# Kernel tuning notes

Measured on AMD Instinct MI355X. Metric: run time of the kernel, lower is better.

## Reference

```python
import math
import jax, jax.numpy as jnp
import numpy as np

WS = (2, 8, 8)   # (D, H, W) window
NUM_HEADS = 8


def get_position_index(ws):
    d, h, w = ws
    coords = jnp.stack(jnp.meshgrid(jnp.arange(d), jnp.arange(h), jnp.arange(w), indexing='ij'))
    cf = coords.reshape(3, -1)                      # [3, N]
    rel = cf[:, :, None] - cf[:, None, :]           # [3, N, N]
    rel = rel.transpose(1, 2, 0)                    # [N, N, 3]
    rel = rel + jnp.array([d - 1, h - 1, w - 1])
    rel = rel * jnp.array([(2 * h - 1) * (2 * w - 1), 2 * w - 1, 1])
    return rel.sum(-1)                              # [N, N] int32


def get_sine_position_encoding(HW, num_pos_feats, temperature=10000.0):
    # normalize=True path of the torch code
    scale = 2 * math.pi
    H, W = HW
    ones = jnp.ones((1, H, W), jnp.float32)
    y = jnp.cumsum(ones, 1)
    x = jnp.cumsum(ones, 2)
    eps = 1e-6
    y = y / (y[:, -1:, :] + eps) * scale
    x = x / (x[:, :, -1:] + eps) * scale
    dim_t = jnp.arange(num_pos_feats)
    dim_t = temperature ** (2.0 * (dim_t // 2).astype(jnp.float32) / num_pos_feats)
    px = x[..., None] / dim_t                       # [1,H,W,F]
    py = y[..., None] / dim_t
    px = jnp.stack((jnp.sin(px[..., 0::2]), jnp.cos(px[..., 1::2])), -1).reshape(1, H, W, num_pos_feats)
    py = jnp.stack((jnp.sin(py[..., 0::2]), jnp.cos(py[..., 1::2])), -1).reshape(1, H, W, num_pos_feats)
    pos = jnp.concatenate((py, px), 3)              # [1,H,W,2F]
    return pos.reshape(1, H * W, 2 * num_pos_feats)  # [1, H*W, C]


def setup_inputs() -> dict:
    key = jax.random.key(0)
    ks = jax.random.split(key, 6)
    B_, N, C = 2048, 128, 256
    return {
        'x': jax.random.normal(ks[0], (B_, N, C), jnp.float32),
        'rpb_table': jax.random.normal(ks[1], (675, NUM_HEADS), jnp.float32) * 0.02,
        'W_qkv_self': jax.random.normal(ks[2], (3 * C, C), jnp.float32) * 0.05,
        'W_qkv_mut': jax.random.normal(ks[3], (3 * C, C), jnp.float32) * 0.05,
        'W_proj': jax.random.normal(ks[4], (C, 2 * C), jnp.float32) * 0.05,
        'b_proj': jax.random.normal(ks[5], (C,), jnp.float32) * 0.05,
    }


def reference(x, rpb_table, W_qkv_self, W_qkv_mut, W_proj, b_proj):
    B, N, C = x.shape
    H = NUM_HEADS
    hd = C // H
    scale = hd ** -0.5

    def qkv_split(y, W):
        qkv = (y @ W.T).reshape(B, N, 3, H, hd).transpose(2, 0, 3, 1, 4)  # [3,B,H,N,hd]
        return qkv[0], qkv[1], qkv[2]

    def attn_fn(q, k, v, bias):
        a = jnp.einsum('bhnd,bhmd->bhnm', q * scale, k)
        if bias is not None:
            a = a + bias
        a = jax.nn.softmax(a, axis=-1)
        o = jnp.einsum('bhnm,bhmd->bhnd', a, v)
        return o.transpose(0, 2, 1, 3).reshape(B, -1, C)

    # self attention with relative position bias
    rpi = get_position_index(WS)                                   # [N,N]
    bias = rpb_table[rpi.reshape(-1)].reshape(N, N, H).transpose(2, 0, 1)[None]  # [1,H,N,N]
    q, k, v = qkv_split(x, W_qkv_self)
    x_out = attn_fn(q, k, v, bias)                                 # [B,N,C]

    # mutual cross-attention between the two frames
    pos = jnp.tile(get_sine_position_encoding(WS[1:], C // 2), (1, 2, 1)).astype(x.dtype)
    q, k, v = qkv_split(x + pos, W_qkv_mut)
    Nh = N // 2
    q1, q2 = q[:, :, :Nh], q[:, :, Nh:]
    k1, k2 = k[:, :, :Nh], k[:, :, Nh:]
    v1, v2 = v[:, :, :Nh], v[:, :, Nh:]
    x1_aligned = attn_fn(q2, k1, v1, None)                         # [B,N/2,C]
    x2_aligned = attn_fn(q1, k2, v2, None)
    x_out = jnp.concatenate([jnp.concatenate([x1_aligned, x2_aligned], 1), x_out], 2)  # [B,N,2C]

    return x_out @ W_proj.T + b_proj                               # [B,N,C]
```

## Files before the change

kernel.cpp:

```cpp
#include <hip/hip_runtime.h>


typedef __attribute__((ext_vector_type(8))) short     short8;
typedef __attribute__((ext_vector_type(8))) __bf16    bf16x8;
typedef __attribute__((ext_vector_type(4))) float     f32x4;

#define LOG2E 1.4426950408889634f

__device__ __forceinline__ unsigned short f2bf(float f) {
  return __builtin_bit_cast(unsigned short, (__bf16)f);
}

__device__ __forceinline__ void gload_lds16(const void* g, void* l) {
  __builtin_amdgcn_global_load_lds((const __attribute__((address_space(1))) void*)g,
                                   (__attribute__((address_space(3))) void*)l, 16, 0, 0);
}


__global__ void pos_kernel(float* __restrict__ pos_t) {
  int e = blockIdx.x * 256 + threadIdx.x;
  int t = e >> 8, c = e & 255;
  int p = t & 63;
  const float norm = 6.28318530717958647692f / 8.000001f;
  float yn = (float)((p >> 3) + 1) * norm;
  float xn = (float)((p & 7) + 1) * norm;
  int cc = c & 127;
  int m  = cc >> 1;
  float v = ((c < 128) ? yn : xn) * __expf(-(float)m * 0.14391156831f);
  pos_t[e] = (cc & 1) ? cosf(v) : sinf(v);
}

__global__ void posw_kernel(const float* __restrict__ pos_t,
                            const float* __restrict__ Wm,
                            float* __restrict__ posW) {
  int e = blockIdx.x * 256 + threadIdx.x;
  int t = e / 768, c = e - t * 768;
  const float4* pr = (const float4*)(pos_t + t * 256);
  const float4* wr = (const float4*)(Wm + (size_t)c * 256);
  float acc = 0.f;
  #pragma unroll 8
  for (int k = 0; k < 64; ++k) {
    float4 p = pr[k], w = wr[k];
    acc += p.x * w.x + p.y * w.y + p.z * w.z + p.w * w.w;
  }
  if (c < 256) acc *= 0.17677669529663688f * LOG2E;
  posW[e] = acc;
}

__global__ void bias_kernel(const float* __restrict__ rpb, float* __restrict__ bias_t) {
  int e = blockIdx.x * 256 + threadIdx.x;
  int h = e >> 14, i = (e >> 7) & 127, j = e & 127;
  int di = i >> 6, hi = (i >> 3) & 7, wi = i & 7;
  int dj = j >> 6, hj = (j >> 3) & 7, wj = j & 7;
  int idx = (di - dj + 1) * 225 + (hi - hj + 7) * 15 + (wi - wj + 7);
  bias_t[e] = rpb[idx * 8 + h] * LOG2E;
}

__global__ void wconv_kernel(const float* __restrict__ Ws, const float* __restrict__ Wm,
                             const float* __restrict__ Wp,
                             unsigned short* __restrict__ Wsb,
                             unsigned short* __restrict__ Wmb,
                             unsigned short* __restrict__ Wpb) {
  int e = blockIdx.x * 256 + threadIdx.x;
  const float qs = 0.17677669529663688f * LOG2E;
  if (e < 196608) {
    float v = Ws[e]; if (e < 65536) v *= qs;
    Wsb[e] = f2bf(v);
  } else if (e < 393216) {
    int i = e - 196608;
    float v = Wm[i]; if (i < 65536) v *= qs;
    Wmb[i] = f2bf(v);
  } else {
    Wpb[e - 393216] = f2bf(Wp[e - 393216]);
  }
}

__global__ void xconv_kernel(const float* __restrict__ x, unsigned short* __restrict__ xb16) {
  for (size_t i8 = ((size_t)blockIdx.x * 256 + threadIdx.x) * 8; i8 < 67108864ull;
       i8 += (size_t)gridDim.x * 256 * 8) {
    float4 a = *(const float4*)(x + i8);
    float4 d = *(const float4*)(x + i8 + 4);
    short8 o;
    o[0] = (short)f2bf(a.x); o[1] = (short)f2bf(a.y);
    o[2] = (short)f2bf(a.z); o[3] = (short)f2bf(a.w);
    o[4] = (short)f2bf(d.x); o[5] = (short)f2bf(d.y);
    o[6] = (short)f2bf(d.z); o[7] = (short)f2bf(d.w);
    *(short8*)(xb16 + i8) = o;
  }
}


template<bool XB>
__global__ __launch_bounds__(512, 4) void qkv_attn(
    const float* __restrict__ xf,
    const unsigned short* __restrict__ xb16,
    const unsigned short* __restrict__ Wsb,
    const unsigned short* __restrict__ Wmb,
    const float* __restrict__ posW,
    const float* __restrict__ bias_t,
    unsigned short* __restrict__ xcat)
{
  __shared__ unsigned short Wl[24576];
  __shared__ unsigned short Qsh[128 * 40];
  __shared__ unsigned short Ksh[128 * 40];
  __shared__ unsigned short VT[32 * 136];
  unsigned short* Psh = Wl;

  const int kblk = blockIdx.x;
  const int b    = (kblk & 7) | ((kblk >> 7) << 3);
  const int g    = (kblk >> 3) & 15;
  const int h    = g >> 1;
  const bool self = (g & 1) == 0;

  const int tid = threadIdx.x, w = tid >> 6, lane = tid & 63;
  const int lr = lane & 15, lk = lane >> 4;
  const unsigned short* Wb = self ? Wsb : Wmb;
  const int m0 = w * 16;

  #pragma unroll
  for (int i = 0; i < 6; ++i) {
    int s  = w * 6 + i;
    int u  = s >> 3, kc = s & 7;
    int o  = u >> 1, nt = u & 1;
    gload_lds16((const char*)Wb + (size_t)(o * 256 + h * 32 + nt * 16 + lr) * 512
                                + kc * 64 + lk * 16,
                (char*)Wl + s * 1024 + lane * 16);
  }

  float pre_r[32];
  if (self) {
    const float* bt = bias_t + (size_t)h * 16384 + (m0 + lk * 4) * 128;
    #pragma unroll
    for (int nf = 0; nf < 8; ++nf)
      #pragma unroll
      for (int r = 0; r < 4; ++r)
        pre_r[nf * 4 + r] = bt[r * 128 + nf * 16 + lr];
  } else {
    #pragma unroll
    for (int u = 0; u < 6; ++u) {
      const int o = u >> 1, nt = u & 1;
      #pragma unroll
      for (int r = 0; r < 4; ++r)
        pre_r[u * 4 + r] = posW[(m0 + lk * 4 + r) * 768 + o * 256 + h * 32 + nt * 16 + lr];
    }
  }

  const float*          xrowf = xf   + (size_t)((b * 128 + m0 + lr) * 256 + lk * 8);
  const unsigned short* xrowb = xb16 + (size_t)((b * 128 + m0 + lr) * 256 + lk * 8);

  float4 xrf[2][2];
  short8 xrb[2];
  if (XB) {
    xrb[0] = *(const short8*)(xrowb);
    xrb[1] = *(const short8*)(xrowb + 32);
  } else {
    xrf[0][0] = *(const float4*)(xrowf);
    xrf[0][1] = *(const float4*)(xrowf + 4);
    xrf[1][0] = *(const float4*)(xrowf + 32);
    xrf[1][1] = *(const float4*)(xrowf + 36);
  }

  __syncthreads();

  f32x4 acc[6];
  #pragma unroll
  for (int u = 0; u < 6; ++u) acc[u] = f32x4{0.f, 0.f, 0.f, 0.f};

  const char* wfrag = (const char*)Wl + lane * 16;

  #pragma unroll
  for (int kc = 0; kc < 8; ++kc) {
    bf16x8 af;
    if (XB) {
      af = __builtin_bit_cast(bf16x8, xrb[kc & 1]);
      if (kc + 2 < 8) xrb[kc & 1] = *(const short8*)(xrowb + (kc + 2) * 32);
    } else {
      float4 a = xrf[kc & 1][0], d = xrf[kc & 1][1];
      if (kc + 2 < 8) {
        xrf[kc & 1][0] = *(const float4*)(xrowf + (kc + 2) * 32);
        xrf[kc & 1][1] = *(const float4*)(xrowf + (kc + 2) * 32 + 4);
      }
      af[0] = (__bf16)a.x; af[1] = (__bf16)a.y; af[2] = (__bf16)a.z; af[3] = (__bf16)a.w;
      af[4] = (__bf16)d.x; af[5] = (__bf16)d.y; af[6] = (__bf16)d.z; af[7] = (__bf16)d.w;
    }
    __builtin_amdgcn_s_setprio(1);
    #pragma unroll
    for (int u = 0; u < 6; ++u) {
      bf16x8 wf = *(const bf16x8*)(wfrag + ((u * 8 + kc) << 10));
      acc[u] = __builtin_amdgcn_mfma_f32_16x16x32_bf16(af, wf, acc[u], 0, 0, 0);
    }
    __builtin_amdgcn_s_setprio(0);
  }

  #pragma unroll
  for (int u = 0; u < 6; ++u) {
    const int o = u >> 1, nt = u & 1;
    #pragma unroll
    for (int r = 0; r < 4; ++r) {
      int row  = m0 + lk * 4 + r;
      int dcol = nt * 16 + lr;
      float v = acc[u][r];
      if (!self) v += pre_r[u * 4 + r];
      if (o == 2)      VT[dcol * 136 + row] = f2bf(v);
      else if (o == 0) Qsh[row * 40 + dcol] = f2bf(v);
      else             Ksh[row * 40 + dcol] = f2bf(v);
    }
  }
  __syncthreads();

  if (self) {
    f32x4 sc[8];
    bf16x8 qa = *(const bf16x8*)&Qsh[(m0 + lr) * 40 + lk * 8];
    __builtin_amdgcn_s_setprio(1);
    #pragma unroll
    for (int nf = 0; nf < 8; ++nf) {
      bf16x8 kb = *(const bf16x8*)&Ksh[(nf * 16 + lr) * 40 + lk * 8];
      sc[nf] = __builtin_amdgcn_mfma_f32_16x16x32_bf16(qa, kb,
                                                       f32x4{0.f,0.f,0.f,0.f}, 0, 0, 0);
    }
    __builtin_amdgcn_s_setprio(0);
    float rsum[4] = {0.f, 0.f, 0.f, 0.f};
    #pragma unroll
    for (int nf = 0; nf < 8; ++nf)
      #pragma unroll
      for (int r = 0; r < 4; ++r) {
        float p = exp2f(sc[nf][r] + pre_r[nf * 4 + r]);
        rsum[r] += p;
        sc[nf][r] = p;
      }
    float rs[4];
    #pragma unroll
    for (int r = 0; r < 4; ++r) {
      float t = rsum[r];
      #pragma unroll
      for (int dd = 1; dd < 16; dd <<= 1) t += __shfl_xor(t, dd, 64);
      rs[r] = 1.f / t;
    }
    f32x4 oc[2];
    oc[0] = f32x4{0.f,0.f,0.f,0.f}; oc[1] = f32x4{0.f,0.f,0.f,0.f};
    #pragma unroll
    for (int c = 0; c < 4; ++c) {
      #pragma unroll
      for (int nf2 = 0; nf2 < 2; ++nf2)
        #pragma unroll
        for (int r = 0; r < 4; ++r)
          Psh[(m0 + lk * 4 + r) * 40 + nf2 * 16 + lr] = f2bf(sc[c * 2 + nf2][r]);
      bf16x8 pa = *(const bf16x8*)&Psh[(m0 + lr) * 40 + lk * 8];
      #pragma unroll
      for (int nt = 0; nt < 2; ++nt) {
        bf16x8 vb = *(const bf16x8*)&VT[(nt * 16 + lr) * 136 + c * 32 + lk * 8];
        oc[nt] = __builtin_amdgcn_mfma_f32_16x16x32_bf16(pa, vb, oc[nt], 0, 0, 0);
      }
    }
    #pragma unroll
    for (int nt = 0; nt < 2; ++nt)
      #pragma unroll
      for (int r = 0; r < 4; ++r) {
        size_t row = (size_t)b * 128 + m0 + lk * 4 + r;
        xcat[row * 512 + 256 + h * 32 + nt * 16 + lr] = f2bf(oc[nt][r] * rs[r]);
      }
  } else {
    const int q0   = (w < 4) ? 64 + m0 : m0 - 64;
    const int koff = (w < 4) ? 0 : 64;
    f32x4 sc2[4];
    bf16x8 qa = *(const bf16x8*)&Qsh[(q0 + lr) * 40 + lk * 8];
    __builtin_amdgcn_s_setprio(1);
    #pragma unroll
    for (int nf = 0; nf < 4; ++nf) {
      bf16x8 kb = *(const bf16x8*)&Ksh[(koff + nf * 16 + lr) * 40 + lk * 8];
      sc2[nf] = __builtin_amdgcn_mfma_f32_16x16x32_bf16(qa, kb,
                                                        f32x4{0.f,0.f,0.f,0.f}, 0, 0, 0);
    }
    __builtin_amdgcn_s_setprio(0);
    float rsum2[4] = {0.f, 0.f, 0.f, 0.f};
    #pragma unroll
    for (int nf = 0; nf < 4; ++nf)
      #pragma unroll
      for (int r = 0; r < 4; ++r) {
        float p = exp2f(sc2[nf][r]);
        rsum2[r] += p;
        sc2[nf][r] = p;
      }
    float rs2[4];
    #pragma unroll
    for (int r = 0; r < 4; ++r) {
      float t = rsum2[r];
      #pragma unroll
      for (int dd = 1; dd < 16; dd <<= 1) t += __shfl_xor(t, dd, 64);
      rs2[r] = 1.f / t;
    }
    f32x4 oc[2];
    oc[0] = f32x4{0.f,0.f,0.f,0.f}; oc[1] = f32x4{0.f,0.f,0.f,0.f};
    #pragma unroll
    for (int c = 0; c < 2; ++c) {
      #pragma unroll
      for (int nf2 = 0; nf2 < 2; ++nf2)
        #pragma unroll
        for (int r = 0; r < 4; ++r)
          Psh[(m0 + lk * 4 + r) * 40 + nf2 * 16 + lr] = f2bf(sc2[c * 2 + nf2][r]);
      bf16x8 pa = *(const bf16x8*)&Psh[(m0 + lr) * 40 + lk * 8];
      #pragma unroll
      for (int nt = 0; nt < 2; ++nt) {
        bf16x8 vb = *(const bf16x8*)&VT[(nt * 16 + lr) * 136 + koff + c * 32 + lk * 8];
        oc[nt] = __builtin_amdgcn_mfma_f32_16x16x32_bf16(pa, vb, oc[nt], 0, 0, 0);
      }
    }
    #pragma unroll
    for (int nt = 0; nt < 2; ++nt)
      #pragma unroll
      for (int r = 0; r < 4; ++r) {
        size_t row = (size_t)b * 128 + m0 + lk * 4 + r;
        xcat[row * 512 + h * 32 + nt * 16 + lr] = f2bf(oc[nt][r] * rs2[r]);
      }
  }
}


__global__ __launch_bounds__(512, 2) void proj_kernel(
    const unsigned short* __restrict__ xcat,
    const unsigned short* __restrict__ Wpb,
    const float* __restrict__ bp,
    float* __restrict__ out)
{
  __shared__ unsigned short Alds[2][128 * 64];
  __shared__ unsigned short Blds[2][256 * 64];

  const int tid = threadIdx.x, w = tid >> 6, lane = tid & 63;
  const int lr = lane & 15, lk = lane >> 4;
  const int wr = w >> 2, wc = w & 3;
  const size_t m0 = (size_t)blockIdx.x * 128;

  f32x4 acc[4][4];
  #pragma unroll
  for (int i = 0; i < 4; ++i)
    #pragma unroll
    for (int j = 0; j < 4; ++j) acc[i][j] = f32x4{0.f, 0.f, 0.f, 0.f};

  auto stage = [&](int buf, int k0) {
    #pragma unroll
    for (int i = 0; i < 2; ++i) {
      int L = (i * 512 + tid) * 16;
      int row = L >> 7;
      int inrow = (L & 127) ^ ((row & 7) << 4);
      gload_lds16((const char*)xcat + (m0 + row) * 1024 + k0 * 2 + inrow,
                  (char*)&Alds[buf][0] + L);
    }
    #pragma unroll
    for (int i = 0; i < 4; ++i) {
      int L = (i * 512 + tid) * 16;
      int row = L >> 7;
      int inrow = (L & 127) ^ ((row & 7) << 4);
      gload_lds16((const char*)Wpb + (size_t)row * 1024 + k0 * 2 + inrow,
                  (char*)&Blds[buf][0] + L);
    }
  };

  stage(0, 0);
  __syncthreads();
  int cur = 0;
  for (int t = 0; t < 8; ++t) {
    if (t < 7) stage(cur ^ 1, (t + 1) * 64);
    const char* At = (const char*)&Alds[cur][0];
    const char* Bt = (const char*)&Blds[cur][0];
    #pragma unroll
    for (int kk = 0; kk < 2; ++kk) {
      bf16x8 af[4], bfr[4];
      #pragma unroll
      for (int mt = 0; mt < 4; ++mt) {
        int row = wr * 64 + mt * 16 + lr;
        int off = (row * 128 + kk * 64 + lk * 16) ^ ((row & 7) << 4);
        af[mt] = *(const bf16x8*)(At + off);
      }
      #pragma unroll
      for (int nt = 0; nt < 4; ++nt) {
        int row = wc * 64 + nt * 16 + lr;
        int off = (row * 128 + kk * 64 + lk * 16) ^ ((row & 7) << 4);
        bfr[nt] = *(const bf16x8*)(Bt + off);
      }
      #pragma unroll
      for (int mt = 0; mt < 4; ++mt)
        #pragma unroll
        for (int nt = 0; nt < 4; ++nt)
          acc[mt][nt] = __builtin_amdgcn_mfma_f32_16x16x32_bf16(af[mt], bfr[nt],
                                                                acc[mt][nt], 0, 0, 0);
    }
    __syncthreads();
    cur ^= 1;
  }

  #pragma unroll
  for (int mt = 0; mt < 4; ++mt)
    #pragma unroll
    for (int r = 0; r < 4; ++r) {
      size_t grow = m0 + wr * 64 + mt * 16 + lk * 4 + r;
      #pragma unroll
      for (int nt = 0; nt < 4; ++nt) {
        int gcol = wc * 64 + nt * 16 + lr;
        out[grow * 256 + gcol] = acc[mt][nt][r] + bp[gcol];
      }
    }
}


extern "C" void kernel_launch(void* const* d_in, const int* in_sizes, int n_in,
                              void* d_out, int out_size, void* d_ws, size_t ws_size,
                              hipStream_t stream) {
  (void)in_sizes; (void)n_in; (void)out_size;
  const float* x   = (const float*)d_in[0];
  const float* rpb = (const float*)d_in[1];
  const float* Wqs = (const float*)d_in[2];
  const float* Wqm = (const float*)d_in[3];
  const float* Wp  = (const float*)d_in[4];
  const float* bp  = (const float*)d_in[5];
  char* ws = (char*)d_ws;

  size_t off = 0;
  float* pos_t  = (float*)(ws + off); off += 32768ull  * 4;
  float* posW   = (float*)(ws + off); off += 98304ull  * 4;
  float* bias_t = (float*)(ws + off); off += 131072ull * 4;
  unsigned short* Wsb = (unsigned short*)(ws + off); off += 196608ull * 2;
  unsigned short* Wmb = (unsigned short*)(ws + off); off += 196608ull * 2;
  unsigned short* Wpb = (unsigned short*)(ws + off); off += 131072ull * 2;
  if (ws_size < off) return;
  unsigned short* xb16 = (unsigned short*)(ws + off);
  const bool use_xb = (ws_size >= off + 67108864ull * 2);

  unsigned short* xcat = (unsigned short*)d_out;

  pos_kernel <<<dim3(128),  dim3(256), 0, stream>>>(pos_t);
  bias_kernel<<<dim3(512),  dim3(256), 0, stream>>>(rpb, bias_t);
  wconv_kernel<<<dim3(2048), dim3(256), 0, stream>>>(Wqs, Wqm, Wp, Wsb, Wmb, Wpb);
  posw_kernel<<<dim3(384),  dim3(256), 0, stream>>>(pos_t, Wqm, posW);

  if (use_xb) {
    xconv_kernel<<<dim3(8192), dim3(256), 0, stream>>>(x, xb16);
    qkv_attn<true><<<dim3(32768), dim3(512), 0, stream>>>(
        x, xb16, Wsb, Wmb, posW, bias_t, xcat);
  } else {
    qkv_attn<false><<<dim3(32768), dim3(512), 0, stream>>>(
        x, xb16, Wsb, Wmb, posW, bias_t, xcat);
  }

  proj_kernel<<<dim3(2048), dim3(512), 0, stream>>>(xcat, Wpb, bp, (float*)d_out);
}
```

Baseline: 834.5 us.

## Split QKV projection into two half-weight phases to halve LDS staging

The fused QKV-plus-attention kernel now stages only half of the per-head weight slice in shared memory at a time. It runs the projection GEMM in two phases of three output tiles each, and reuses the buffer between them. The aim is to cut shared-memory use and accumulator registers so more workgroups fit per CU. In exchange it adds two extra barriers, re-reads the x rows for the second phase, and serialises the second weight load behind the first GEMM. The reused Wl buffer also backs Psh, so its smaller size must still fit the probability tile.

```diff
diff --git a/kernel.cpp b/kernel.cpp
--- a/kernel.cpp
+++ b/kernel.cpp
@@ -100,7 +100,7 @@
     const float* __restrict__ bias_t,
     unsigned short* __restrict__ xcat)
 {
-  __shared__ unsigned short Wl[24576];
+  __shared__ unsigned short Wl[12288];
   __shared__ unsigned short Qsh[128 * 40];
   __shared__ unsigned short Ksh[128 * 40];
   __shared__ unsigned short VT[32 * 136];
@@ -117,95 +117,125 @@
   const unsigned short* Wb = self ? Wsb : Wmb;
   const int m0 = w * 16;
 
-  #pragma unroll
-  for (int i = 0; i < 6; ++i) {
-    int s  = w * 6 + i;
-    int u  = s >> 3, kc = s & 7;
-    int o  = u >> 1, nt = u & 1;
-    gload_lds16((const char*)Wb + (size_t)(o * 256 + h * 32 + nt * 16 + lr) * 512
-                                + kc * 64 + lk * 16,
-                (char*)Wl + s * 1024 + lane * 16);
-  }
-
-  float pre_r[32];
-  if (self) {
-    const float* bt = bias_t + (size_t)h * 16384 + (m0 + lk * 4) * 128;
-    #pragma unroll
-    for (int nf = 0; nf < 8; ++nf)
-      #pragma unroll
-      for (int r = 0; r < 4; ++r)
-        pre_r[nf * 4 + r] = bt[r * 128 + nf * 16 + lr];
-  } else {
-    #pragma unroll
-    for (int u = 0; u < 6; ++u) {
-      const int o = u >> 1, nt = u & 1;
-      #pragma unroll
-      for (int r = 0; r < 4; ++r)
-        pre_r[u * 4 + r] = posW[(m0 + lk * 4 + r) * 768 + o * 256 + h * 32 + nt * 16 + lr];
-    }
-  }
+  auto stageW = [&](int ub) {
+    #pragma unroll
+    for (int i = 0; i < 3; ++i) {
+      int s  = w * 3 + i;
+      int ul = s >> 3, kc = s & 7;
+      int u  = ub + ul;
+      int o  = u >> 1, nt = u & 1;
+      gload_lds16((const char*)Wb + (size_t)(o * 256 + h * 32 + nt * 16 + lr) * 512
+                                  + kc * 64 + lk * 16,
+                  (char*)Wl + s * 1024 + lane * 16);
+    }
+  };
 
   const float*          xrowf = xf   + (size_t)((b * 128 + m0 + lr) * 256 + lk * 8);
   const unsigned short* xrowb = xb16 + (size_t)((b * 128 + m0 + lr) * 256 + lk * 8);
-
+  const char* wfrag = (const char*)Wl + lane * 16;
+
+  short8 xrb[2];
   float4 xrf[2][2];
-  short8 xrb[2];
-  if (XB) {
-    xrb[0] = *(const short8*)(xrowb);
-    xrb[1] = *(const short8*)(xrowb + 32);
-  } else {
-    xrf[0][0] = *(const float4*)(xrowf);
-    xrf[0][1] = *(const float4*)(xrowf + 4);
-    xrf[1][0] = *(const float4*)(xrowf + 32);
-    xrf[1][1] = *(const float4*)(xrowf + 36);
-  }
-
-  __syncthreads();
-
-  f32x4 acc[6];
-  #pragma unroll
-  for (int u = 0; u < 6; ++u) acc[u] = f32x4{0.f, 0.f, 0.f, 0.f};
-
-  const char* wfrag = (const char*)Wl + lane * 16;
-
-  #pragma unroll
-  for (int kc = 0; kc < 8; ++kc) {
-    bf16x8 af;
+  auto xpre = [&]() {
     if (XB) {
-      af = __builtin_bit_cast(bf16x8, xrb[kc & 1]);
-      if (kc + 2 < 8) xrb[kc & 1] = *(const short8*)(xrowb + (kc + 2) * 32);
+      xrb[0] = *(const short8*)(xrowb);
+      xrb[1] = *(const short8*)(xrowb + 32);
     } else {
-      float4 a = xrf[kc & 1][0], d = xrf[kc & 1][1];
-      if (kc + 2 < 8) {
-        xrf[kc & 1][0] = *(const float4*)(xrowf + (kc + 2) * 32);
-        xrf[kc & 1][1] = *(const float4*)(xrowf + (kc + 2) * 32 + 4);
-      }
-      af[0] = (__bf16)a.x; af[1] = (__bf16)a.y; af[2] = (__bf16)a.z; af[3] = (__bf16)a.w;
-      af[4] = (__bf16)d.x; af[5] = (__bf16)d.y; af[6] = (__bf16)d.z; af[7] = (__bf16)d.w;
-    }
-    __builtin_amdgcn_s_setprio(1);
-    #pragma unroll
-    for (int u = 0; u < 6; ++u) {
-      bf16x8 wf = *(const bf16x8*)(wfrag + ((u * 8 + kc) << 10));
-      acc[u] = __builtin_amdgcn_mfma_f32_16x16x32_bf16(af, wf, acc[u], 0, 0, 0);
-    }
-    __builtin_amdgcn_s_setprio(0);
-  }
-
-  #pragma unroll
-  for (int u = 0; u < 6; ++u) {
+      xrf[0][0] = *(const float4*)(xrowf);
+      xrf[0][1] = *(const float4*)(xrowf + 4);
+      xrf[1][0] = *(const float4*)(xrowf + 32);
+      xrf[1][1] = *(const float4*)(xrowf + 36);
+    }
+  };
+  auto kloop = [&](f32x4 acc[3]) {
+    #pragma unroll
+    for (int kc = 0; kc < 8; ++kc) {
+      bf16x8 af;
+      if (XB) {
+        af = __builtin_bit_cast(bf16x8, xrb[kc & 1]);
+        if (kc + 2 < 8) xrb[kc & 1] = *(const short8*)(xrowb + (kc + 2) * 32);
+      } else {
+        float4 a = xrf[kc & 1][0], d = xrf[kc & 1][1];
+        if (kc + 2 < 8) {
+          xrf[kc & 1][0] = *(const float4*)(xrowf + (kc + 2) * 32);
+          xrf[kc & 1][1] = *(const float4*)(xrowf + (kc + 2) * 32 + 4);
+        }
+        af[0] = (__bf16)a.x; af[1] = (__bf16)a.y; af[2] = (__bf16)a.z; af[3] = (__bf16)a.w;
+        af[4] = (__bf16)d.x; af[5] = (__bf16)d.y; af[6] = (__bf16)d.z; af[7] = (__bf16)d.w;
+      }
+      __builtin_amdgcn_s_setprio(1);
+      #pragma unroll
+      for (int ul = 0; ul < 3; ++ul) {
+        bf16x8 wf = *(const bf16x8*)(wfrag + ((ul * 8 + kc) << 10));
+        acc[ul] = __builtin_amdgcn_mfma_f32_16x16x32_bf16(af, wf, acc[ul], 0, 0, 0);
+      }
+      __builtin_amdgcn_s_setprio(0);
+    }
+  };
+  auto epi = [&](int u, const f32x4& a, const float* pr) {
     const int o = u >> 1, nt = u & 1;
     #pragma unroll
     for (int r = 0; r < 4; ++r) {
       int row  = m0 + lk * 4 + r;
       int dcol = nt * 16 + lr;
-      float v = acc[u][r];
-      if (!self) v += pre_r[u * 4 + r];
+      float v = a[r];
+      if (!self) v += pr[r];
       if (o == 2)      VT[dcol * 136 + row] = f2bf(v);
       else if (o == 0) Qsh[row * 40 + dcol] = f2bf(v);
       else             Ksh[row * 40 + dcol] = f2bf(v);
     }
-  }
+  };
+
+  stageW(0);
+  float pre0[12];
+  if (!self) {
+    #pragma unroll
+    for (int u = 0; u < 3; ++u) {
+      const int o = u >> 1, nt = u & 1;
+      #pragma unroll
+      for (int r = 0; r < 4; ++r)
+        pre0[u * 4 + r] = posW[(m0 + lk * 4 + r) * 768 + o * 256 + h * 32 + nt * 16 + lr];
+    }
+  }
+  xpre();
+  __syncthreads();
+
+  f32x4 acc[3];
+  acc[0] = f32x4{0.f,0.f,0.f,0.f}; acc[1] = f32x4{0.f,0.f,0.f,0.f};
+  acc[2] = f32x4{0.f,0.f,0.f,0.f};
+  kloop(acc);
+  __syncthreads();
+
+  stageW(3);
+  xpre();
+  float pre1[32];
+  if (self) {
+    const float* bt = bias_t + (size_t)h * 16384 + (m0 + lk * 4) * 128;
+    #pragma unroll
+    for (int nf = 0; nf < 8; ++nf)
+      #pragma unroll
+      for (int r = 0; r < 4; ++r)
+        pre1[nf * 4 + r] = bt[r * 128 + nf * 16 + lr];
+  } else {
+    #pragma unroll
+    for (int u = 3; u < 6; ++u) {
+      const int o = u >> 1, nt = u & 1;
+      #pragma unroll
+      for (int r = 0; r < 4; ++r)
+        pre1[(u - 3) * 4 + r] = posW[(m0 + lk * 4 + r) * 768 + o * 256 + h * 32 + nt * 16 + lr];
+    }
+  }
+  epi(0, acc[0], pre0 + 0);
+  epi(1, acc[1], pre0 + 4);
+  epi(2, acc[2], pre0 + 8);
+  __syncthreads();
+
+  acc[0] = f32x4{0.f,0.f,0.f,0.f}; acc[1] = f32x4{0.f,0.f,0.f,0.f};
+  acc[2] = f32x4{0.f,0.f,0.f,0.f};
+  kloop(acc);
+  epi(3, acc[0], pre1 + 0);
+  epi(4, acc[1], pre1 + 4);
+  epi(5, acc[2], pre1 + 8);
   __syncthreads();
 
   if (self) {
@@ -224,7 +254,7 @@
     for (int nf = 0; nf < 8; ++nf)
       #pragma unroll
       for (int r = 0; r < 4; ++r) {
-        float p = exp2f(sc[nf][r] + pre_r[nf * 4 + r]);
+        float p = exp2f(sc[nf][r] + pre1[nf * 4 + r]);
         rsum[r] += p;
         sc[nf][r] = p;
       }
```

New measurement: 1.066 ms. 27.7% more time.
